# Kernel optimization log

Measured on AMD Instinct MI355X. Metric: run time of the kernel, lower is better.

The kernel has to match this reference:

```python
import jax, jax.numpy as jnp
import numpy as np

N, C, A = 4096, 1000, 64


def setup_inputs() -> dict:
    key = jax.random.key(0)
    k1, k2, k3, k4, k5 = jax.random.split(key, 5)
    weight_m = jax.random.normal(k1, (C, A), dtype=jnp.float32)
    y = jax.random.normal(k2, (N, C), dtype=jnp.float32)
    features = jax.random.normal(k3, (N, A), dtype=jnp.float32)
    target_x = jax.random.randint(k4, (N,), 0, C)
    ratio = jnp.float32(0.5)
    final_conv = jax.random.normal(k5, (N, A, A), dtype=jnp.float32) * 0.1
    return {
        "weight_m": weight_m,
        "y": y,
        "features": features,
        "target_x": target_x,
        "ratio": ratio,
        "final_conv": final_conv,
        "class_num": C,
    }


def reference(weight_m, y, features, target_x, ratio, final_conv, class_num):
    # weight_m: (C, A); y: (N, C); features: (N, A) (only supplies N, A)
    # target_x: (N,) int labels; final_conv: (N, A, A); ratio: scalar
    Wk = weight_m[target_x]                       # (N, A)  gather of label row
    d = weight_m[None, :, :] - Wk[:, None, :]     # (N, C, A) = NxW_ij - NxW_kj

    # sigma1 = ||w_j||^2 - ||w_{y_n}||^2
    w2 = jnp.sum(weight_m * weight_m, axis=-1)    # (C,)
    sigma1 = w2[None, :] - w2[target_x][:, None]  # (N, C)

    # sigma2 = ratio * diag(d @ CV @ d^T), computed directly (no NxCxC matrix)
    t = jnp.einsum('nca,nab->ncb', d, final_conv)  # (N, C, A)
    sigma2 = ratio * jnp.sum(t * d, axis=-1)       # (N, C)

    logits = y + 0.5 * sigma2 + sigma1             # (N, C)

    # mean cross-entropy (nn.CrossEntropyLoss default)
    logp = jax.nn.log_softmax(logits, axis=-1)
    nll = -jnp.take_along_axis(logp, target_x[:, None], axis=1)[:, 0]
    loss = jnp.mean(nll)
    return loss, y
```

## Files before the change

### kernel.cpp

```cpp
#include <hip/hip_runtime.h>
#include <hip/hip_bf16.h>
#include <stdint.h>
#include <stddef.h>

#define N_    4096
#define C_    1000
#define CP    1024
#define A_    64
#define KPACK 2080
#define KCROSS (KPACK + 64)
#define KTOT  2176
#define KSPLIT 1152
#define MS    68

typedef __bf16 bf16_8 __attribute__((ext_vector_type(8)));
typedef float  f32_4  __attribute__((ext_vector_type(4)));
typedef int    i32_4  __attribute__((ext_vector_type(4)));
typedef int    i32_8  __attribute__((ext_vector_type(8)));

__device__ __forceinline__ void gl2lds16(const void* g, void* l) {
  __builtin_amdgcn_global_load_lds(
      (const __attribute__((address_space(1))) void*)g,
      (__attribute__((address_space(3))) void*)l, 16, 0, 0);
}

__device__ __forceinline__ uint16_t pk_fp8(float a, float b) {
  return (uint16_t)(__builtin_amdgcn_cvt_pk_fp8_f32(a, b, 0, false) & 0xffff);
}

__device__ __forceinline__ void unpack_pair(int k, int& a, int& b) {
  a = (int)(0.5f * (129.0f - sqrtf((float)(16641 - 8 * k))));
  if (a < 0) a = 0;
  while ((a + 1) * (129 - (a + 1)) / 2 <= k) ++a;
  while (a * (129 - a) / 2 > k) --a;
  b = k - a * (129 - a) / 2 + a;
}

__global__ __launch_bounds__(256) void prep_all(
    const float* __restrict__ W, const int* __restrict__ tgt,
    const float* __restrict__ CV, uint8_t* __restrict__ Bo,
    float* __restrict__ w2, uint8_t* __restrict__ Aq, float* __restrict__ qn) {
  __shared__ float Ms[64 * MS];
  __shared__ float up[4 * 64];
  __shared__ float wk[64];
  __shared__ float us[64];
  int t = threadIdx.x;

  if (blockIdx.x < 1024) {
    int c = blockIdx.x;
    float* ws = Ms;
    if (t < 64) {
      float w = (c < C_) ? W[c * 64 + t] : 0.f;
      ws[t] = w;
      float s = w * w;
      for (int o = 32; o; o >>= 1) s += __shfl_down(s, o);
      if (t == 0 && c < C_) w2[c] = s;
    }
    __syncthreads();
    uint8_t* row = Bo + (size_t)c * KTOT;
    for (int p = t; p < KPACK / 2; p += 256) {
      int k = 2 * p;
      int a0, b0, a1, b1;
      unpack_pair(k, a0, b0);
      if (b0 == 63) { a1 = a0 + 1; b1 = a1; } else { a1 = a0; b1 = b0 + 1; }
      *(uint16_t*)(row + k) = pk_fp8(ws[a0] * ws[b0], ws[a1] * ws[b1]);
    }
    if (t < 32) *(uint16_t*)(row + KPACK + 2 * t) = pk_fp8(ws[2 * t], ws[2 * t + 1]);
    if (t >= 32 && t < 48) *(uint16_t*)(row + KCROSS + 2 * (t - 32)) = 0;
  } else {
    int n = blockIdx.x - 1024;
    int lbl = tgt[n];
    if (t < 64) wk[t] = W[lbl * 64 + t];
    const float4* M4 = (const float4*)(CV + (size_t)n * 4096);
    for (int j = 0; j < 4; ++j) {
      int i4 = t + j * 256;
      int r = i4 >> 4, c4 = (i4 & 15) << 2;
      *(float4*)&Ms[r * MS + c4] = M4[i4];
    }
    __syncthreads();
    {
      int a = t & 63, seg = t >> 6;
      float acc = 0.f;
      for (int b = seg * 16; b < seg * 16 + 16; ++b)
        acc += (Ms[a * MS + b] + Ms[b * MS + a]) * wk[b];
      up[seg * 64 + a] = acc;
    }
    __syncthreads();
    if (t < 64) {
      float u = up[t] + up[64 + t] + up[128 + t] + up[192 + t];
      us[t] = u;
      float p = wk[t] * u;
      for (int o = 32; o; o >>= 1) p += __shfl_down(p, o);
      if (t == 0) qn[n] = 0.5f * p;
    }
    __syncthreads();
    uint8_t* row = Aq + (size_t)n * KTOT;
    for (int p = t; p < KPACK / 2; p += 256) {
      int k = 2 * p;
      int a0, b0, a1, b1;
      unpack_pair(k, a0, b0);
      if (b0 == 63) { a1 = a0 + 1; b1 = a1; } else { a1 = a0; b1 = b0 + 1; }
      float v0 = (a0 == b0) ? Ms[a0 * MS + a0] : (Ms[a0 * MS + b0] + Ms[b0 * MS + a0]);
      float v1 = (a1 == b1) ? Ms[a1 * MS + a1] : (Ms[a1 * MS + b1] + Ms[b1 * MS + a1]);
      *(uint16_t*)(row + k) = pk_fp8(v0, v1);
    }
    if (t < 32) *(uint16_t*)(row + KPACK + 2 * t) = pk_fp8(-us[2 * t], -us[2 * t + 1]);
    if (t >= 32 && t < 48) *(uint16_t*)(row + KCROSS + 2 * (t - 32)) = 0;
  }
}

#define BM 64
#define BN 128
#define BK 128
__global__ __launch_bounds__(256) void gemm_s(const uint8_t* __restrict__ Aq,
                                              const uint8_t* __restrict__ Bo,
                                              __bf16* __restrict__ Sbase) {
  __shared__ uint8_t As[BM * BK];
  __shared__ uint8_t Bs[BN * BK];
  int t = threadIdx.x;
  int lane = t & 63;
  int w = t >> 6;
  int wr = w & 1;
  int wc = w >> 1;
  int rowBase = blockIdx.x * BM;
  int colBase = blockIdx.y * BN;
  int kb = blockIdx.z ? KSPLIT : 0;
  int ke = blockIdx.z ? KTOT : KSPLIT;
  __bf16* S = Sbase + (size_t)blockIdx.z * ((size_t)N_ * CP);

  f32_4 acc[2][4];
  for (int mi = 0; mi < 2; ++mi)
    for (int ni = 0; ni < 4; ++ni)
      acc[mi][ni] = (f32_4){0.f, 0.f, 0.f, 0.f};

  int m0 = lane & 15;
  int q = lane >> 4;
  int sw = m0 & 7;
  int c0 = ((2 * q) ^ sw) << 4;
  int c1 = ((2 * q + 1) ^ sw) << 4;

  for (int k0 = kb; k0 < ke; k0 += BK) {
    __syncthreads();
    for (int r = 0; r < 2; ++r) {
      int ch = r * 256 + t;
      int row_p = ch >> 3, qp = ch & 7;
      int q_log = qp ^ (row_p & 7);
      const uint8_t* g = Aq + (size_t)(rowBase + row_p) * KTOT + k0 + (q_log << 4);
      gl2lds16(g, As + ch * 16);
    }
    for (int r = 0; r < 4; ++r) {
      int ch = r * 256 + t;
      int row_p = ch >> 3, qp = ch & 7;
      int q_log = qp ^ (row_p & 7);
      const uint8_t* g = Bo + (size_t)(colBase + row_p) * KTOT + k0 + (q_log << 4);
      gl2lds16(g, Bs + ch * 16);
    }
    __syncthreads();
    i32_8 af[2], bf[4];
    for (int mi = 0; mi < 2; ++mi) {
      const uint8_t* base = &As[(wr * 32 + mi * 16 + m0) * BK];
      i32_4 lo = *(const i32_4*)(base + c0);
      i32_4 hi = *(const i32_4*)(base + c1);
      af[mi] = __builtin_shufflevector(lo, hi, 0, 1, 2, 3, 4, 5, 6, 7);
    }
    for (int ni = 0; ni < 4; ++ni) {
      const uint8_t* base = &Bs[(wc * 64 + ni * 16 + m0) * BK];
      i32_4 lo = *(const i32_4*)(base + c0);
      i32_4 hi = *(const i32_4*)(base + c1);
      bf[ni] = __builtin_shufflevector(lo, hi, 0, 1, 2, 3, 4, 5, 6, 7);
    }
    for (int mi = 0; mi < 2; ++mi)
      for (int ni = 0; ni < 4; ++ni)
        acc[mi][ni] = __builtin_amdgcn_mfma_scale_f32_16x16x128_f8f6f4(
            bf[ni], af[mi], acc[mi][ni], 0, 0,
            0, 0x7F7F7F7F, 0, 0x7F7F7F7F);
  }

  int ll = lane & 15;
  int lh = lane >> 4;
  for (int mi = 0; mi < 2; ++mi) {
    int n0 = rowBase + wr * 32 + mi * 16 + ll;
    for (int ni = 0; ni < 4; ++ni) {
      int cc0 = colBase + wc * 64 + ni * 16 + lh * 4;
      union { __bf16 h[4]; uint2 u; } pk;
      for (int j = 0; j < 4; ++j) pk.h[j] = (__bf16)acc[mi][ni][j];
      *(uint2*)&S[(size_t)n0 * CP + cc0] = pk.u;
    }
  }
}

__global__ __launch_bounds__(256) void epilogue(
    const __bf16* __restrict__ Sb, const float* __restrict__ y,
    const float* __restrict__ w2, const float* __restrict__ qn,
    const int* __restrict__ tgt, const float* __restrict__ ratio_p,
    float* __restrict__ nll, float* __restrict__ outy) {
  int t = threadIdx.x, lane = t & 63, w = t >> 6;
  int n = blockIdx.x * 4 + w;
  float hr = 0.5f * (*ratio_p);
  int lbl = tgt[n];
  float q = qn[n];
  float w2k = w2[lbl];
  const bf16_8* S0 = (const bf16_8*)(Sb + (size_t)n * CP);
  const bf16_8* S1 = (const bf16_8*)(Sb + 1ull * N_ * CP + (size_t)n * CP);
  const float* yr = y + (size_t)n * C_;
  float* oy = outy + (size_t)n * C_;
  float l[16];
  float mx = -1e30f;
  for (int i = 0; i < 2; ++i) {
    int idx = i * 64 + lane;
    bf16_8 a0 = S0[idx], a1 = S1[idx];
    int c0 = idx * 8;
    for (int j = 0; j < 8; ++j) {
      int c = c0 + j;
      float v = -1e30f;
      if (c < C_) {
        float s = (float)a0[j] + (float)a1[j];
        v = yr[c] + (w2[c] - w2k) + hr * (s + q);
      }
      l[i * 8 + j] = v;
      mx = fmaxf(mx, v);
    }
  }
  for (int c = lane; c < C_; c += 64) oy[c] = yr[c];
  for (int o = 32; o; o >>= 1) mx = fmaxf(mx, __shfl_xor(mx, o));
  float se = 0.f, lt = 0.f;
  for (int i = 0; i < 2; ++i) {
    int c0 = (i * 64 + lane) * 8;
    for (int j = 0; j < 8; ++j) {
      float v = l[i * 8 + j];
      se += expf(v - mx);
      lt += (c0 + j == lbl) ? v : 0.f;
    }
  }
  for (int o = 32; o; o >>= 1) {
    se += __shfl_xor(se, o);
    lt += __shfl_xor(lt, o);
  }
  if (lane == 0) nll[n] = (mx + logf(se)) - lt;
}

__global__ void reduce_loss(const float* __restrict__ nll, float* __restrict__ out) {
  int t = threadIdx.x;
  float s = 0.f;
  for (int i = t; i < N_; i += 256) s += nll[i];
  for (int o = 32; o; o >>= 1) s += __shfl_down(s, o);
  __shared__ float r[4];
  if ((t & 63) == 0) r[t >> 6] = s;
  __syncthreads();
  if (t == 0) out[0] = (r[0] + r[1] + r[2] + r[3]) * (1.0f / (float)N_);
}

extern "C" void kernel_launch(void* const* d_in, const int* in_sizes, int n_in,
                              void* d_out, int out_size, void* d_ws, size_t ws_size,
                              hipStream_t stream) {
  const float* W     = (const float*)d_in[0];
  const float* y     = (const float*)d_in[1];
  const int*   tgt   = (const int*)d_in[3];
  const float* ratio = (const float*)d_in[4];
  const float* CV    = (const float*)d_in[5];

  char* ws = (char*)d_ws;
  size_t off = 0;
  uint8_t* Aq = (uint8_t*)(ws + off); off += (size_t)N_ * KTOT;
  uint8_t* Bo = (uint8_t*)(ws + off); off += (size_t)CP * KTOT;
  __bf16* S   = (__bf16*)(ws + off);  off += 2ull * N_ * CP * sizeof(__bf16);
  float* w2   = (float*)(ws + off);   off += 4096;
  float* qn   = (float*)(ws + off);   off += (size_t)N_ * sizeof(float);
  float* nll  = (float*)(ws + off);   off += (size_t)N_ * sizeof(float);

  float* out = (float*)d_out;

  prep_all<<<1024 + N_, 256, 0, stream>>>(W, tgt, CV, Bo, w2, Aq, qn);
  gemm_s<<<dim3(N_ / BM, CP / BN, 2), 256, 0, stream>>>(Aq, Bo, S);
  epilogue<<<N_ / 4, 256, 0, stream>>>(S, y, w2, qn, tgt, ratio, nll, out + 1);
  reduce_loss<<<1, 256, 0, stream>>>(nll, out);
}
```

Measured before the change: 164.6 us.

## Use constexpr pair table, fold loss reduction into epilogue, pad LDS stride

Replaces the sqrt-and-loop triangular index unpacking with a compile-time lookup table of packed (a,b) pairs, so each thread does one 32-bit load instead. The separate single-block reduce_loss launch is removed: the last epilogue block, found through an atomic counter that prep_all resets, sums nll and writes the mean. The LDS row stride for the covariance tile also changes from 68 to 72. The aim is to cut ALU work in prep and one kernel launch, at the cost of atomic and fence overhead in every epilogue block.

```diff
diff --git a/kernel.cpp b/kernel.cpp
--- a/kernel.cpp
+++ b/kernel.cpp
@@ -11,7 +11,7 @@
 #define KCROSS (KPACK + 64)
 #define KTOT  2176
 #define KSPLIT 1152
-#define MS    68
+#define MS    72
 
 typedef __bf16 bf16_8 __attribute__((ext_vector_type(8)));
 typedef float  f32_4  __attribute__((ext_vector_type(4)));
@@ -28,23 +28,28 @@
   return (uint16_t)(__builtin_amdgcn_cvt_pk_fp8_f32(a, b, 0, false) & 0xffff);
 }
 
-__device__ __forceinline__ void unpack_pair(int k, int& a, int& b) {
-  a = (int)(0.5f * (129.0f - sqrtf((float)(16641 - 8 * k))));
-  if (a < 0) a = 0;
-  while ((a + 1) * (129 - (a + 1)) / 2 <= k) ++a;
-  while (a * (129 - a) / 2 > k) --a;
-  b = k - a * (129 - a) / 2 + a;
-}
+struct PairTab { uint16_t v[KPACK]; };
+constexpr PairTab make_tab() {
+  PairTab t{};
+  int k = 0;
+  for (int a = 0; a < 64; ++a)
+    for (int b = a; b < 64; ++b) { t.v[k] = (uint16_t)((a << 8) | b); ++k; }
+  return t;
+}
+__device__ constexpr PairTab PT = make_tab();
 
 __global__ __launch_bounds__(256) void prep_all(
     const float* __restrict__ W, const int* __restrict__ tgt,
     const float* __restrict__ CV, uint8_t* __restrict__ Bo,
-    float* __restrict__ w2, uint8_t* __restrict__ Aq, float* __restrict__ qn) {
+    float* __restrict__ w2, uint8_t* __restrict__ Aq, float* __restrict__ qn,
+    int* __restrict__ cnt) {
   __shared__ float Ms[64 * MS];
   __shared__ float up[4 * 64];
   __shared__ float wk[64];
   __shared__ float us[64];
   int t = threadIdx.x;
+
+  if (blockIdx.x == 0 && t == 0) *cnt = 0;
 
   if (blockIdx.x < 1024) {
     int c = blockIdx.x;
@@ -60,9 +65,9 @@
     uint8_t* row = Bo + (size_t)c * KTOT;
     for (int p = t; p < KPACK / 2; p += 256) {
       int k = 2 * p;
-      int a0, b0, a1, b1;
-      unpack_pair(k, a0, b0);
-      if (b0 == 63) { a1 = a0 + 1; b1 = a1; } else { a1 = a0; b1 = b0 + 1; }
+      uint32_t pr = *(const uint32_t*)&PT.v[k];
+      int b0 = pr & 255, a0 = (pr >> 8) & 255;
+      int b1 = (pr >> 16) & 255, a1 = (pr >> 24) & 255;
       *(uint16_t*)(row + k) = pk_fp8(ws[a0] * ws[b0], ws[a1] * ws[b1]);
     }
     if (t < 32) *(uint16_t*)(row + KPACK + 2 * t) = pk_fp8(ws[2 * t], ws[2 * t + 1]);
@@ -97,9 +102,9 @@
     uint8_t* row = Aq + (size_t)n * KTOT;
     for (int p = t; p < KPACK / 2; p += 256) {
       int k = 2 * p;
-      int a0, b0, a1, b1;
-      unpack_pair(k, a0, b0);
-      if (b0 == 63) { a1 = a0 + 1; b1 = a1; } else { a1 = a0; b1 = b0 + 1; }
+      uint32_t pr = *(const uint32_t*)&PT.v[k];
+      int b0 = pr & 255, a0 = (pr >> 8) & 255;
+      int b1 = (pr >> 16) & 255, a1 = (pr >> 24) & 255;
       float v0 = (a0 == b0) ? Ms[a0 * MS + a0] : (Ms[a0 * MS + b0] + Ms[b0 * MS + a0]);
       float v1 = (a1 == b1) ? Ms[a1 * MS + a1] : (Ms[a1 * MS + b1] + Ms[b1 * MS + a1]);
       *(uint16_t*)(row + k) = pk_fp8(v0, v1);
@@ -193,7 +198,8 @@
     const __bf16* __restrict__ Sb, const float* __restrict__ y,
     const float* __restrict__ w2, const float* __restrict__ qn,
     const int* __restrict__ tgt, const float* __restrict__ ratio_p,
-    float* __restrict__ nll, float* __restrict__ outy) {
+    float* __restrict__ nll, float* __restrict__ outy,
+    float* __restrict__ out0, int* __restrict__ cnt) {
   int t = threadIdx.x, lane = t & 63, w = t >> 6;
   int n = blockIdx.x * 4 + w;
   float hr = 0.5f * (*ratio_p);
@@ -237,17 +243,25 @@
     lt += __shfl_xor(lt, o);
   }
   if (lane == 0) nll[n] = (mx + logf(se)) - lt;
-}
-
-__global__ void reduce_loss(const float* __restrict__ nll, float* __restrict__ out) {
-  int t = threadIdx.x;
-  float s = 0.f;
-  for (int i = t; i < N_; i += 256) s += nll[i];
-  for (int o = 32; o; o >>= 1) s += __shfl_down(s, o);
-  __shared__ float r[4];
-  if ((t & 63) == 0) r[t >> 6] = s;
+
   __syncthreads();
-  if (t == 0) out[0] = (r[0] + r[1] + r[2] + r[3]) * (1.0f / (float)N_);
+  __shared__ int lastf;
+  if (t == 0) {
+    __threadfence();
+    int old = atomicAdd(cnt, 1);
+    lastf = (old == (int)gridDim.x - 1);
+  }
+  __syncthreads();
+  if (lastf) {
+    __threadfence();
+    float s = 0.f;
+    for (int i = t; i < N_; i += 256) s += nll[i];
+    for (int o = 32; o; o >>= 1) s += __shfl_down(s, o);
+    __shared__ float r[4];
+    if ((t & 63) == 0) r[t >> 6] = s;
+    __syncthreads();
+    if (t == 0) out0[0] = (r[0] + r[1] + r[2] + r[3]) * (1.0f / (float)N_);
+  }
 }
 
 extern "C" void kernel_launch(void* const* d_in, const int* in_sizes, int n_in,
@@ -267,11 +281,11 @@
   float* w2   = (float*)(ws + off);   off += 4096;
   float* qn   = (float*)(ws + off);   off += (size_t)N_ * sizeof(float);
   float* nll  = (float*)(ws + off);   off += (size_t)N_ * sizeof(float);
+  int*   cnt  = (int*)(ws + off);     off += 256;
 
   float* out = (float*)d_out;
 
-  prep_all<<<1024 + N_, 256, 0, stream>>>(W, tgt, CV, Bo, w2, Aq, qn);
+  prep_all<<<1024 + N_, 256, 0, stream>>>(W, tgt, CV, Bo, w2, Aq, qn, cnt);
   gemm_s<<<dim3(N_ / BM, CP / BN, 2), 256, 0, stream>>>(Aq, Bo, S);
-  epilogue<<<N_ / 4, 256, 0, stream>>>(S, y, w2, qn, tgt, ratio, nll, out + 1);
-  reduce_loss<<<1, 256, 0, stream>>>(nll, out);
-}
+  epilogue<<<N_ / 4, 256, 0, stream>>>(S, y, w2, qn, tgt, ratio, nll, out + 1, out, cnt);
+}
```

Result: slower. 189.4 us (+15.0%).
